# Optimization experiments

Hardware: AMD Instinct MI355X
Metric: run time of the kernel (lower is better)

## Reference

```python
import jax, jax.numpy as jnp
import numpy as np

N_NODES = 100000
N_EDGES = 1600000
D_IN = 128
D_OUT = 128


def setup_inputs() -> dict:
    key = jax.random.key(0)
    k1, k2, k3, k4 = jax.random.split(key, 4)
    x = jax.random.normal(k1, (N_NODES, D_IN), dtype=jnp.float32)
    # Xavier-uniform-like init for weight (exact distribution irrelevant for correctness baseline)
    weight = jax.random.normal(k2, (D_IN, D_OUT), dtype=jnp.float32) * (1.0 / np.sqrt(D_IN))
    bias = jnp.zeros((D_OUT,), dtype=jnp.float32)
    edge_index = jax.random.randint(k3, (2, N_EDGES), 0, N_NODES, dtype=jnp.int64 if jax.config.read('jax_enable_x64') else jnp.int32)
    edge_weight = jax.random.uniform(k4, (N_EDGES,), dtype=jnp.float32)
    return {"x": x, "weight": weight, "bias": bias,
            "edge_index": edge_index, "edge_weight": edge_weight}


def reference(x, weight, bias, edge_index, edge_weight):
    # support = X @ W   -- dense projection [N, D_out]
    support = x @ weight
    # output = A @ support -- SpMM via gather + weighted segment-sum
    src = edge_index[1]  # column index of adj (neighbor being aggregated)
    dst = edge_index[0]  # row index of adj (node receiving the message)
    messages = support[src] * edge_weight[:, None]          # [E, D_out]
    out = jax.ops.segment_sum(messages, dst, num_segments=N_NODES)  # [N, D_out]
    return out + bias
```

## Files before the change

### kernel.cpp

```cpp
#include <hip/hip_runtime.h>
#include <hip/hip_bf16.h>

#define N_NODES 100000
#define N_EDGES 1600000
#define D 128

#define NBUK 1024
#define BSH 7
#define CAP 2560
#define CAP_H 1344
#define NAGG2 (((N_NODES + 127) >> BSH) * 2)
#define NSCAT 256
#define PA_EPB 6250
#define NGB ((N_NODES / 16 + 15) / 16)
#define SRC_MASK 0x01FFFFFF

typedef __attribute__((ext_vector_type(8))) short bf16x8;
typedef __attribute__((ext_vector_type(4))) float f32x4;

static __device__ __forceinline__ short f2bf(float f) {
    unsigned u = __builtin_bit_cast(unsigned, f);
    u += 0x7FFFu + ((u >> 16) & 1u);
    return (short)(u >> 16);
}
static __device__ __forceinline__ float bf2f(unsigned short h) {
    unsigned u = ((unsigned)h) << 16;
    return __builtin_bit_cast(float, u);
}

__global__ void wt_kernel(const float* __restrict__ w, short* __restrict__ wt,
                          int* __restrict__ gcur) {
    const int i = blockIdx.x * blockDim.x + threadIdx.x;
    if (i < D * D) {
        const int k = i / D, c = i % D;
        wt[c * D + k] = f2bf(w[i]);
    }
    if (i < NBUK) gcur[i] = 0;
}

__global__ __launch_bounds__(1024, 8) void gemm_scatter_kernel(
    const float* __restrict__ x, const short* __restrict__ wt,
    short* __restrict__ sup, const int* __restrict__ dst,
    const int* __restrict__ src, const float* __restrict__ ew,
    int* __restrict__ gcur, int2* __restrict__ inter_sw) {
    __shared__ int h[NBUK];
    const int t = threadIdx.x;

    if (blockIdx.x < NSCAT) {
        if (t < NBUK) h[t] = 0;
        __syncthreads();
        const int beg = blockIdx.x * PA_EPB;
        const int end = min(beg + PA_EPB, N_EDGES);
        for (int i = beg + t; i < end; i += 1024)
            atomicAdd(&h[dst[i] >> BSH], 1);
        __syncthreads();
        if (t < NBUK) {
            const int c = h[t];
            h[t] = c ? (t * CAP + atomicAdd(&gcur[t], c)) : 0;
        }
        __syncthreads();
        for (int i = beg + t; i < end; i += 1024) {
            const int d = dst[i];
            const int pos = atomicAdd(&h[d >> BSH], 1);
            inter_sw[pos] = make_int2(src[i] | ((d & 127) << 25),
                                      __float_as_int(ew[i]));
        }
        return;
    }

    const int wid = (blockIdx.x - NSCAT) * 16 + (t >> 6);
    if (wid >= N_NODES / 16) return;
    const int l = t & 63;
    const int r = l & 15, g = l >> 4;
    const size_t row0 = (size_t)wid * 16;

    bf16x8 a[4];
    const float* xp = x + (row0 + r) * D + g * 8;
#pragma unroll
    for (int ks = 0; ks < 4; ++ks) {
        const float4 f0 = *reinterpret_cast<const float4*>(xp + ks * 32);
        const float4 f1 = *reinterpret_cast<const float4*>(xp + ks * 32 + 4);
        bf16x8 tt;
        tt[0] = f2bf(f0.x); tt[1] = f2bf(f0.y); tt[2] = f2bf(f0.z); tt[3] = f2bf(f0.w);
        tt[4] = f2bf(f1.x); tt[5] = f2bf(f1.y); tt[6] = f2bf(f1.z); tt[7] = f2bf(f1.w);
        a[ks] = tt;
    }

#pragma unroll
    for (int nt = 0; nt < 8; ++nt) {
        f32x4 acc = {0.f, 0.f, 0.f, 0.f};
        const short* wp = wt + (size_t)(nt * 16 + r) * D + g * 8;
#pragma unroll
        for (int ks = 0; ks < 4; ++ks) {
            const bf16x8 b = *reinterpret_cast<const bf16x8*>(wp + ks * 32);
            acc = __builtin_amdgcn_mfma_f32_16x16x32_bf16(a[ks], b, acc, 0, 0, 0);
        }
        short* sp = sup + (row0 + g * 4) * D + nt * 16 + r;
#pragma unroll
        for (int q = 0; q < 4; ++q) sp[q * D] = f2bf(acc[q]);
    }
}

__global__ __launch_bounds__(512) void sortagg_kernel(
    const int* __restrict__ gcur, const int2* __restrict__ inter_sw,
    const short* __restrict__ sup, const float* __restrict__ bias,
    float* __restrict__ out) {
    __shared__ int2 eb[CAP_H];
    __shared__ int st[64];
    __shared__ int cur[64];
    const int b = blockIdx.x, t = threadIdx.x;
    const int cb = b >> 1, hf = b & 1;
    const int cnt = gcur[cb];
    const int2* in = inter_sw + (size_t)cb * CAP;

    if (t < 64) st[t] = 0;
    __syncthreads();

    int2 e0, e1, e2, e3, e4;
    bool k0 = false, k1 = false, k2 = false, k3 = false, k4 = false;
    const int i0 = t, i1 = t + 512, i2 = t + 1024, i3 = t + 1536, i4 = t + 2048;
    if (i0 < cnt) { e0 = in[i0]; const int d7 = (unsigned)e0.x >> 25; if ((d7 >> 6) == hf) { k0 = true; atomicAdd(&st[d7 & 63], 1); } }
    if (i1 < cnt) { e1 = in[i1]; const int d7 = (unsigned)e1.x >> 25; if ((d7 >> 6) == hf) { k1 = true; atomicAdd(&st[d7 & 63], 1); } }
    if (i2 < cnt) { e2 = in[i2]; const int d7 = (unsigned)e2.x >> 25; if ((d7 >> 6) == hf) { k2 = true; atomicAdd(&st[d7 & 63], 1); } }
    if (i3 < cnt) { e3 = in[i3]; const int d7 = (unsigned)e3.x >> 25; if ((d7 >> 6) == hf) { k3 = true; atomicAdd(&st[d7 & 63], 1); } }
    if (i4 < cnt) { e4 = in[i4]; const int d7 = (unsigned)e4.x >> 25; if ((d7 >> 6) == hf) { k4 = true; atomicAdd(&st[d7 & 63], 1); } }
    __syncthreads();

    if (t < 64) {
        const int hv = st[t];
        int s = hv;
#pragma unroll
        for (int o = 1; o < 64; o <<= 1) {
            const int v = __shfl_up(s, o);
            if (t >= o) s += v;
        }
        st[t] = s - hv;
        cur[t] = s - hv;
    }
    __syncthreads();

    if (k0) eb[atomicAdd(&cur[((unsigned)e0.x >> 25) & 63], 1)] = make_int2(e0.x & SRC_MASK, e0.y);
    if (k1) eb[atomicAdd(&cur[((unsigned)e1.x >> 25) & 63], 1)] = make_int2(e1.x & SRC_MASK, e1.y);
    if (k2) eb[atomicAdd(&cur[((unsigned)e2.x >> 25) & 63], 1)] = make_int2(e2.x & SRC_MASK, e2.y);
    if (k3) eb[atomicAdd(&cur[((unsigned)e3.x >> 25) & 63], 1)] = make_int2(e3.x & SRC_MASK, e3.y);
    if (k4) eb[atomicAdd(&cur[((unsigned)e4.x >> 25) & 63], 1)] = make_int2(e4.x & SRC_MASK, e4.y);
    __syncthreads();

    const int wv = t >> 6, lane = t & 63;
    const int g = lane >> 4;
    const int fl = lane & 15;
    const int node0 = (cb << BSH) + (hf << 6);

    const float4 b0 = *reinterpret_cast<const float4*>(&bias[fl * 8]);
    const float4 b1 = *reinterpret_cast<const float4*>(&bias[fl * 8 + 4]);

    for (int k = 0; k < 8; ++k) {
        const int nl = wv * 8 + k;
        const int node = node0 + nl;
        if (node >= N_NODES) break;
        const int beg = st[nl], end = cur[nl];

        float acc[8] = {0, 0, 0, 0, 0, 0, 0, 0};
        for (int i = beg + g; i < end; i += 4) {
            const int2 sw = eb[i];
            const float w = __int_as_float(sw.y);
            const bf16x8 v = *reinterpret_cast<const bf16x8*>(
                &sup[(size_t)sw.x * D + fl * 8]);
#pragma unroll
            for (int q = 0; q < 8; ++q)
                acc[q] = fmaf(w, bf2f((unsigned short)v[q]), acc[q]);
        }
#pragma unroll
        for (int q = 0; q < 8; ++q) {
            acc[q] += __shfl_xor(acc[q], 16);
            acc[q] += __shfl_xor(acc[q], 32);
        }
        if (g == 0) {
            float* o = &out[(size_t)node * D + fl * 8];
            reinterpret_cast<float4*>(o)[0] =
                make_float4(acc[0] + b0.x, acc[1] + b0.y, acc[2] + b0.z, acc[3] + b0.w);
            reinterpret_cast<float4*>(o)[1] =
                make_float4(acc[4] + b1.x, acc[5] + b1.y, acc[6] + b1.z, acc[7] + b1.w);
        }
    }
}

extern "C" void kernel_launch(void* const* d_in, const int* in_sizes, int n_in,
                              void* d_out, int out_size, void* d_ws, size_t ws_size,
                              hipStream_t stream) {
    const float* x      = (const float*)d_in[0];
    const float* weight = (const float*)d_in[1];
    const float* bias   = (const float*)d_in[2];
    const int*   eidx   = (const int*)d_in[3];
    const float* ew     = (const float*)d_in[4];
    float* out = (float*)d_out;

    const int* dst_idx = eidx;
    const int* src_idx = eidx + N_EDGES;

    char* p = (char*)d_ws;
    short* sup       = (short*)p;  p += (size_t)N_NODES * D * 2;
    short* wt        = (short*)p;  p += (size_t)D * D * 2;
    int*   gcur      = (int*)p;    p += NBUK * 4;
    int2*  inter_sw  = (int2*)p;   p += (size_t)NBUK * CAP * 8;

    wt_kernel<<<(D * D + 255) / 256, 256, 0, stream>>>(weight, wt, gcur);

    gemm_scatter_kernel<<<NSCAT + NGB, 1024, 0, stream>>>(
        x, wt, sup, dst_idx, src_idx, ew, gcur, inter_sw);

    sortagg_kernel<<<NAGG2, 512, 0, stream>>>(gcur, inter_sw, sup, bias, out);
}
```

Measured before the change: 130.6 us.

## Split fused GEMM/scatter kernel into separate GEMM and bucket-scatter launches

Before, one kernel ran both the bucket scatter of edges and the MFMA projection, with different block roles. Now they are two kernels: a 256-thread MFMA GEMM kernel and a 1024-thread bucket-scatter kernel that uses twice as many blocks, each with half the edges. This removes the heterogeneous-block imbalance and the shared-memory and launch-bounds constraints the fused kernel carried. In exchange, the two phases no longer overlap on the GPU and there is one extra launch.

```diff
diff --git a/kernel.cpp b/kernel.cpp
--- a/kernel.cpp
+++ b/kernel.cpp
@@ -10,9 +10,8 @@
 #define CAP 2560
 #define CAP_H 1344
 #define NAGG2 (((N_NODES + 127) >> BSH) * 2)
-#define NSCAT 256
-#define PA_EPB 6250
-#define NGB ((N_NODES / 16 + 15) / 16)
+#define NSCAT 512
+#define PA_EPB 3125
 #define SRC_MASK 0x01FFFFFF
 
 typedef __attribute__((ext_vector_type(8))) short bf16x8;
@@ -38,39 +37,12 @@
     if (i < NBUK) gcur[i] = 0;
 }
 
-__global__ __launch_bounds__(1024, 8) void gemm_scatter_kernel(
+__global__ __launch_bounds__(256) void gemm_mfma_kernel(
     const float* __restrict__ x, const short* __restrict__ wt,
-    short* __restrict__ sup, const int* __restrict__ dst,
-    const int* __restrict__ src, const float* __restrict__ ew,
-    int* __restrict__ gcur, int2* __restrict__ inter_sw) {
-    __shared__ int h[NBUK];
-    const int t = threadIdx.x;
-
-    if (blockIdx.x < NSCAT) {
-        if (t < NBUK) h[t] = 0;
-        __syncthreads();
-        const int beg = blockIdx.x * PA_EPB;
-        const int end = min(beg + PA_EPB, N_EDGES);
-        for (int i = beg + t; i < end; i += 1024)
-            atomicAdd(&h[dst[i] >> BSH], 1);
-        __syncthreads();
-        if (t < NBUK) {
-            const int c = h[t];
-            h[t] = c ? (t * CAP + atomicAdd(&gcur[t], c)) : 0;
-        }
-        __syncthreads();
-        for (int i = beg + t; i < end; i += 1024) {
-            const int d = dst[i];
-            const int pos = atomicAdd(&h[d >> BSH], 1);
-            inter_sw[pos] = make_int2(src[i] | ((d & 127) << 25),
-                                      __float_as_int(ew[i]));
-        }
-        return;
-    }
-
-    const int wid = (blockIdx.x - NSCAT) * 16 + (t >> 6);
+    short* __restrict__ sup) {
+    const int wid = blockIdx.x * 4 + (threadIdx.x >> 6);
     if (wid >= N_NODES / 16) return;
-    const int l = t & 63;
+    const int l = threadIdx.x & 63;
     const int r = l & 15, g = l >> 4;
     const size_t row0 = (size_t)wid * 16;
 
@@ -80,10 +52,10 @@
     for (int ks = 0; ks < 4; ++ks) {
         const float4 f0 = *reinterpret_cast<const float4*>(xp + ks * 32);
         const float4 f1 = *reinterpret_cast<const float4*>(xp + ks * 32 + 4);
-        bf16x8 tt;
-        tt[0] = f2bf(f0.x); tt[1] = f2bf(f0.y); tt[2] = f2bf(f0.z); tt[3] = f2bf(f0.w);
-        tt[4] = f2bf(f1.x); tt[5] = f2bf(f1.y); tt[6] = f2bf(f1.z); tt[7] = f2bf(f1.w);
-        a[ks] = tt;
+        bf16x8 t;
+        t[0] = f2bf(f0.x); t[1] = f2bf(f0.y); t[2] = f2bf(f0.z); t[3] = f2bf(f0.w);
+        t[4] = f2bf(f1.x); t[5] = f2bf(f1.y); t[6] = f2bf(f1.z); t[7] = f2bf(f1.w);
+        a[ks] = t;
     }
 
 #pragma unroll
@@ -98,6 +70,32 @@
         short* sp = sup + (row0 + g * 4) * D + nt * 16 + r;
 #pragma unroll
         for (int q = 0; q < 4; ++q) sp[q * D] = f2bf(acc[q]);
+    }
+}
+
+__global__ __launch_bounds__(1024) void bukscatter_kernel(
+    const int* __restrict__ dst, const int* __restrict__ src,
+    const float* __restrict__ ew, int* __restrict__ gcur,
+    int2* __restrict__ inter_sw) {
+    __shared__ int h[NBUK];
+    const int t = threadIdx.x;
+    if (t < NBUK) h[t] = 0;
+    __syncthreads();
+    const int beg = blockIdx.x * PA_EPB;
+    const int end = min(beg + PA_EPB, N_EDGES);
+    for (int i = beg + t; i < end; i += 1024)
+        atomicAdd(&h[dst[i] >> BSH], 1);
+    __syncthreads();
+    if (t < NBUK) {
+        const int c = h[t];
+        h[t] = c ? (t * CAP + atomicAdd(&gcur[t], c)) : 0;
+    }
+    __syncthreads();
+    for (int i = beg + t; i < end; i += 1024) {
+        const int d = dst[i];
+        const int pos = atomicAdd(&h[d >> BSH], 1);
+        inter_sw[pos] = make_int2(src[i] | ((d & 127) << 25),
+                                  __float_as_int(ew[i]));
     }
 }
 
@@ -206,8 +204,10 @@
 
     wt_kernel<<<(D * D + 255) / 256, 256, 0, stream>>>(weight, wt, gcur);
 
-    gemm_scatter_kernel<<<NSCAT + NGB, 1024, 0, stream>>>(
-        x, wt, sup, dst_idx, src_idx, ew, gcur, inter_sw);
+    gemm_mfma_kernel<<<(N_NODES / 16 + 3) / 4, 256, 0, stream>>>(x, wt, sup);
+
+    bukscatter_kernel<<<NSCAT, 1024, 0, stream>>>(dst_idx, src_idx, ew, gcur,
+                                                  inter_sw);
 
     sortagg_kernel<<<NAGG2, 512, 0, stream>>>(gcur, inter_sw, sup, bias, out);
 }
```

Result: slower. 134.2 us (+2.8%).
